# Kernel tuning notes

Hardware: AMD Instinct MI355X
Metric: run time of the kernel (lower is better)

## Reference

```python
import jax, jax.numpy as jnp
import numpy as np

B, S, H = 8, 1024, 768
NH, DH = 12, 64
F, E = 3072, 8
EPS = 1e-12

def layer_norm(x, g, b):
    mu = jnp.mean(x, axis=-1, keepdims=True)
    var = jnp.var(x, axis=-1, keepdims=True)
    return g * (x - mu) / jnp.sqrt(var + EPS) + b

def setup_inputs():
    key = jax.random.key(0)
    ks = jax.random.split(key, 20)
    std = 0.02
    d = {
        'hidden_states': jax.random.normal(ks[0], (B, S, H), jnp.float32),
        'Wq': jax.random.normal(ks[1], (H, H)) * std, 'bq': jnp.zeros((H,)),
        'Wk': jax.random.normal(ks[2], (H, H)) * std, 'bk': jnp.zeros((H,)),
        'Wv': jax.random.normal(ks[3], (H, H)) * std, 'bv': jnp.zeros((H,)),
        'Wao': jax.random.normal(ks[4], (H, H)) * std, 'bao': jnp.zeros((H,)),
        'ln1_g': jnp.ones((H,)), 'ln1_b': jnp.zeros((H,)),
        'Wr': jax.random.normal(ks[5], (H, E)) * std, 'br': jnp.zeros((E,)),
        'Wi': jax.random.normal(ks[6], (E, H, F)) * std, 'bi': jnp.zeros((E, F)),
        'Wo': jax.random.normal(ks[7], (F, H)) * std, 'bo': jnp.zeros((H,)),
        'ln2_g': jnp.ones((H,)), 'ln2_b': jnp.zeros((H,)),
    }
    return d

def reference(hidden_states, Wq, bq, Wk, bk, Wv, bv, Wao, bao, ln1_g, ln1_b,
              Wr, br, Wi, bi, Wo, bo, ln2_g, ln2_b):
    b, s, h = hidden_states.shape
    # --- self attention ---
    q = (hidden_states @ Wq + bq).reshape(b, s, NH, DH)
    k = (hidden_states @ Wk + bk).reshape(b, s, NH, DH)
    v = (hidden_states @ Wv + bv).reshape(b, s, NH, DH)
    scores = jnp.einsum('bqhd,bkhd->bhqk', q, k) / jnp.sqrt(jnp.float32(DH))
    probs = jax.nn.softmax(scores, axis=-1)
    ctx = jnp.einsum('bhqk,bkhd->bqhd', probs, v).reshape(b, s, h)
    attention_output = layer_norm(ctx @ Wao + bao + hidden_states, ln1_g, ln1_b)
    # --- router ---
    routing_scores = jax.nn.softmax(attention_output @ Wr + br, axis=-1)  # [b,s,E]
    routing_expert = jnp.argmax(routing_scores, axis=-1)  # [b,s]
    # --- expert FFN (dispatch/combine via per-expert masking) ---
    flat_x = attention_output.reshape(-1, h)          # [T,H]
    flat_e = routing_expert.reshape(-1)               # [T]
    flat_inter = jnp.zeros((b * s, F), flat_x.dtype)
    for e in range(E):
        mask = (flat_e == e)[:, None].astype(flat_x.dtype)
        y = jax.nn.gelu(flat_x @ Wi[e] + bi[e], approximate=False)
        flat_inter = flat_inter + mask * y
    inter = flat_inter.reshape(b, s, F)
    # --- output (dense + residual layernorm) ---
    layer_output = layer_norm(inter @ Wo + bo + attention_output, ln2_g, ln2_b)
    return layer_output, routing_scores
```

## Files before the change

### kernel.cpp

```cpp
#include <hip/hip_runtime.h>
#include <math.h>
#include <stdint.h>

#define TOKS 8192
#define HDIM 768
#define FDIM 3072
#define NEXP 8
#define NHEAD 12
#define SEQ 1024
#define BATCH 8
#define PERMSZ 9216

typedef __attribute__((ext_vector_type(8))) short s16x8;
typedef __attribute__((ext_vector_type(4))) short s16x4;
typedef __attribute__((ext_vector_type(4))) float f32x4;

__device__ __forceinline__ short f2bf(float f) {
  uint32_t u = __float_as_uint(f);
  uint32_t r = (u + 0x7fffu + ((u >> 16) & 1u)) >> 16;
  return (short)(r & 0xffffu);
}
__device__ __forceinline__ float bf2f(short h) {
  return __uint_as_float(((uint32_t)(uint16_t)h) << 16);
}
__device__ __forceinline__ void gload16(const void* g, void* l) {
  __builtin_amdgcn_global_load_lds(
      (const __attribute__((address_space(1))) uint32_t*)g,
      (__attribute__((address_space(3))) uint32_t*)l, 16, 0, 0);
}
__device__ __forceinline__ void pipe_wait_barrier() {
  asm volatile("s_waitcnt vmcnt(0)" ::: "memory");
  __builtin_amdgcn_s_barrier();
}

__global__ __launch_bounds__(256) void convert_split(
    const float* __restrict__ X, short* __restrict__ Xh, short* __restrict__ Xl, int n4)
{
  const int i = blockIdx.x * 256 + threadIdx.x;
  if (i >= n4) return;
  const float4 v = ((const float4*)X)[i];
  const float a[4] = {v.x, v.y, v.z, v.w};
  s16x4 h, l;
#pragma unroll
  for (int j = 0; j < 4; ++j) {
    h[j] = f2bf(a[j]);
    l[j] = f2bf(a[j] - bf2f(h[j]));
  }
  ((s16x4*)Xh)[i] = h;
  ((s16x4*)Xl)[i] = l;
}

__global__ __launch_bounds__(256) void transpose_split(
    const float* __restrict__ W, short* __restrict__ WTh, short* __restrict__ WTl,
    int K, int N)
{
  __shared__ float t[32][33];
  const int tid = threadIdx.x;
  const int tx = tid & 31, ty = tid >> 5;
  const int n0 = blockIdx.x * 32, k0 = blockIdx.y * 32;
#pragma unroll
  for (int r = 0; r < 4; ++r)
    t[ty + r * 8][tx] = W[(size_t)(k0 + ty + r * 8) * N + n0 + tx];
  __syncthreads();
#pragma unroll
  for (int r = 0; r < 4; ++r) {
    const float v = t[tx][ty + r * 8];
    const short h = f2bf(v);
    WTh[(size_t)(n0 + ty + r * 8) * K + k0 + tx] = h;
    WTl[(size_t)(n0 + ty + r * 8) * K + k0 + tx] = f2bf(v - bf2f(h));
  }
}

__global__ __launch_bounds__(256) void qkv_split_mfma(
    const short* __restrict__ Ah, const short* __restrict__ Al,
    const short* __restrict__ BhT, const short* __restrict__ BlT,
    const float* __restrict__ bias,
    short* __restrict__ QKh, short* __restrict__ QKl,
    short* __restrict__ VTh, short* __restrict__ VTl)
{
  const int K = 768;
  __shared__ __align__(16) short lAh[2][4096];
  __shared__ __align__(16) short lAl[2][4096];
  __shared__ __align__(16) short lBh[2][4096];
  __shared__ __align__(16) short lBl[2][4096];
  const int tid = threadIdx.x;
  const int w = tid >> 6, lane = tid & 63;
  const int wr = w >> 1, wc = w & 1;
  const int row0 = blockIdx.y * 128, col0 = blockIdx.x * 128;
  const int sr = lane & 15, kg = lane >> 4;
  const size_t a0 = (size_t)(row0 + 2 * w * 16 + sr) * K + kg * 8;
  const size_t a1 = a0 + (size_t)16 * K;
  const size_t b0 = (size_t)(col0 + 2 * w * 16 + sr) * K + kg * 8;
  const size_t b1 = b0 + (size_t)16 * K;
  const int d0 = (2 * w) * 512, d1 = (2 * w + 1) * 512;
#define STAGE_Q(bu, k0) do { \
    gload16(Ah + a0 + (k0), &lAh[bu][d0]); \
    gload16(Ah + a1 + (k0), &lAh[bu][d1]); \
    gload16(Al + a0 + (k0), &lAl[bu][d0]); \
    gload16(Al + a1 + (k0), &lAl[bu][d1]); \
    gload16(BhT + b0 + (k0), &lBh[bu][d0]); \
    gload16(BhT + b1 + (k0), &lBh[bu][d1]); \
    gload16(BlT + b0 + (k0), &lBl[bu][d0]); \
    gload16(BlT + b1 + (k0), &lBl[bu][d1]); \
  } while (0)
  f32x4 acc[4][4] = {};
  STAGE_Q(0, 0);
  pipe_wait_barrier();
  int cur = 0;
  for (int t = 0; t < 24; ++t) {
    if (t < 23) STAGE_Q(cur ^ 1, (t + 1) * 32);
    s16x8 ah[4], al[4], bh[4], bl[4];
#pragma unroll
    for (int i = 0; i < 4; ++i) {
      ah[i] = *(const s16x8*)&lAh[cur][(wr * 4 + i) * 512 + lane * 8];
      al[i] = *(const s16x8*)&lAl[cur][(wr * 4 + i) * 512 + lane * 8];
      bh[i] = *(const s16x8*)&lBh[cur][(wc * 4 + i) * 512 + lane * 8];
      bl[i] = *(const s16x8*)&lBl[cur][(wc * 4 + i) * 512 + lane * 8];
    }
#pragma unroll
    for (int mi = 0; mi < 4; ++mi)
#pragma unroll
      for (int ni = 0; ni < 4; ++ni) {
        acc[mi][ni] = __builtin_amdgcn_mfma_f32_16x16x32_bf16(ah[mi], bh[ni], acc[mi][ni], 0, 0, 0);
        acc[mi][ni] = __builtin_amdgcn_mfma_f32_16x16x32_bf16(ah[mi], bl[ni], acc[mi][ni], 0, 0, 0);
        acc[mi][ni] = __builtin_amdgcn_mfma_f32_16x16x32_bf16(al[mi], bh[ni], acc[mi][ni], 0, 0, 0);
      }
    pipe_wait_barrier();
    cur ^= 1;
  }
#undef STAGE_Q
  const int cl = lane & 15, rg = lane >> 4;
#pragma unroll
  for (int mi = 0; mi < 4; ++mi)
#pragma unroll
    for (int ni = 0; ni < 4; ++ni) {
      const int c = col0 + wc * 64 + ni * 16 + cl;
      const int rowb = row0 + wr * 64 + mi * 16 + rg * 4;
      s16x4 hv, lv;
#pragma unroll
      for (int r = 0; r < 4; ++r) {
        const float v = acc[mi][ni][r] + bias[c];
        const short hh = f2bf(v);
        hv[r] = hh;
        lv[r] = f2bf(v - bf2f(hh));
      }
      if (c < 1536) {
#pragma unroll
        for (int r = 0; r < 4; ++r) {
          QKh[(size_t)(rowb + r) * 1536 + c] = hv[r];
          QKl[(size_t)(rowb + r) * 1536 + c] = lv[r];
        }
      } else {
        const int dall = c - 1536;
        const size_t vi = (((size_t)((rowb >> 10) * NHEAD + (dall >> 6))) * 64 + (dall & 63)) * 1024
                          + (rowb & 1023);
        *(s16x4*)(VTh + vi) = hv;
        *(s16x4*)(VTl + vi) = lv;
      }
    }
}

__global__ __launch_bounds__(256) void gemm_splitk_staged(
    const short* __restrict__ Ah, const short* __restrict__ Al,
    const short* __restrict__ BhT, const short* __restrict__ BlT,
    const float* __restrict__ bias, float* __restrict__ C0, float* __restrict__ C1,
    int N, int K)
{
  __shared__ __align__(16) short lAh[2][4096];
  __shared__ __align__(16) short lAl[2][4096];
  __shared__ __align__(16) short lBh[2][4096];
  __shared__ __align__(16) short lBl[2][4096];
  const int tid = threadIdx.x;
  const int w = tid >> 6, lane = tid & 63;
  const int wr = w >> 1, wc = w & 1;
  const int row0 = blockIdx.y * 128, col0 = blockIdx.x * 128;
  const int z = blockIdx.z;
  const int Khalf = K >> 1, koff = z * Khalf;
  const int sr = lane & 15, kg = lane >> 4;
  const size_t a0 = (size_t)(row0 + 2 * w * 16 + sr) * K + koff + kg * 8;
  const size_t a1 = a0 + (size_t)16 * K;
  const size_t b0 = (size_t)(col0 + 2 * w * 16 + sr) * K + koff + kg * 8;
  const size_t b1 = b0 + (size_t)16 * K;
  const int d0 = (2 * w) * 512, d1 = (2 * w + 1) * 512;
#define STAGE_K4(bu, k0) do { \
    gload16(Ah + a0 + (k0), &lAh[bu][d0]); \
    gload16(Ah + a1 + (k0), &lAh[bu][d1]); \
    gload16(Al + a0 + (k0), &lAl[bu][d0]); \
    gload16(Al + a1 + (k0), &lAl[bu][d1]); \
    gload16(BhT + b0 + (k0), &lBh[bu][d0]); \
    gload16(BhT + b1 + (k0), &lBh[bu][d1]); \
    gload16(BlT + b0 + (k0), &lBl[bu][d0]); \
    gload16(BlT + b1 + (k0), &lBl[bu][d1]); \
  } while (0)
  f32x4 acc[4][4] = {};
  const int NT = Khalf >> 5;
  STAGE_K4(0, 0);
  pipe_wait_barrier();
  int cur = 0;
  for (int t = 0; t < NT; ++t) {
    if (t + 1 < NT) STAGE_K4(cur ^ 1, (t + 1) * 32);
    s16x8 ah[4], al[4], bh[4], bl[4];
#pragma unroll
    for (int i = 0; i < 4; ++i) {
      ah[i] = *(const s16x8*)&lAh[cur][(wr * 4 + i) * 512 + lane * 8];
      al[i] = *(const s16x8*)&lAl[cur][(wr * 4 + i) * 512 + lane * 8];
      bh[i] = *(const s16x8*)&lBh[cur][(wc * 4 + i) * 512 + lane * 8];
      bl[i] = *(const s16x8*)&lBl[cur][(wc * 4 + i) * 512 + lane * 8];
    }
#pragma unroll
    for (int mi = 0; mi < 4; ++mi)
#pragma unroll
      for (int ni = 0; ni < 4; ++ni) {
        acc[mi][ni] = __builtin_amdgcn_mfma_f32_16x16x32_bf16(ah[mi], bh[ni], acc[mi][ni], 0, 0, 0);
        acc[mi][ni] = __builtin_amdgcn_mfma_f32_16x16x32_bf16(ah[mi], bl[ni], acc[mi][ni], 0, 0, 0);
        acc[mi][ni] = __builtin_amdgcn_mfma_f32_16x16x32_bf16(al[mi], bh[ni], acc[mi][ni], 0, 0, 0);
      }
    pipe_wait_barrier();
    cur ^= 1;
  }
#undef STAGE_K4
  float* C = z ? C1 : C0;
  const int cl = lane & 15, rg = lane >> 4;
#pragma unroll
  for (int mi = 0; mi < 4; ++mi)
#pragma unroll
    for (int r = 0; r < 4; ++r) {
      const int row = row0 + wr * 64 + mi * 16 + rg * 4 + r;
#pragma unroll
      for (int ni = 0; ni < 4; ++ni) {
        const int c = col0 + wc * 64 + ni * 16 + cl;
        C[(size_t)row * N + c] = acc[mi][ni][r] + (z ? 0.f : bias[c]);
      }
    }
}

__global__ __launch_bounds__(256, 2) void attention_part(
    const short* __restrict__ QKh, const short* __restrict__ QKl,
    const short* __restrict__ VTh, const short* __restrict__ VTl,
    float* __restrict__ O0, float* __restrict__ O1,
    float2* __restrict__ ml0, float2* __restrict__ ml1)
{
  __shared__ __align__(16) short lPh[4][2560];
  __shared__ __align__(16) short lPl[4][2560];
  const int tid = threadIdx.x;
  const int w = tid >> 6, lane = tid & 63;
  const int b = blockIdx.z, h = blockIdx.y;
  const int z = blockIdx.x & 1;
  const int q0 = (blockIdx.x >> 1) * 128 + w * 32;
  const int kv0 = z * 512;
  const int sr = lane & 15, kg = lane >> 4;
  const int cl = sr, rg = kg;
  short* myPh = lPh[w];
  short* myPl = lPl[w];
  float* Op = z ? O1 : O0;
  float2* mlp = z ? ml1 : ml0;

  s16x8 qh[2][2], ql[2][2];
  {
    const size_t qbase = ((size_t)b * SEQ + q0 + sr) * 1536 + h * 64 + kg * 8;
#pragma unroll
    for (int mi = 0; mi < 2; ++mi)
#pragma unroll
      for (int ks = 0; ks < 2; ++ks) {
        const size_t o = qbase + (size_t)mi * (16 * 1536) + ks * 32;
        qh[mi][ks] = *(const s16x8*)(QKh + o);
        ql[mi][ks] = *(const s16x8*)(QKl + o);
      }
  }
  float m_run[2][4], l_run[2][4];
#pragma unroll
  for (int mi = 0; mi < 2; ++mi)
#pragma unroll
    for (int r = 0; r < 4; ++r) { m_run[mi][r] = -3.0e38f; l_run[mi][r] = 0.f; }
  f32x4 acc_o[2][4] = {};

  for (int kt = kv0; kt < kv0 + 512; kt += 64) {
    s16x8 kh[4][2], kl2[4][2];
    {
      const size_t kbase = ((size_t)b * SEQ + kt + sr) * 1536 + 768 + h * 64 + kg * 8;
#pragma unroll
      for (int ni = 0; ni < 4; ++ni)
#pragma unroll
        for (int ks = 0; ks < 2; ++ks) {
          const size_t o = kbase + (size_t)ni * (16 * 1536) + ks * 32;
          kh[ni][ks] = *(const s16x8*)(QKh + o);
          kl2[ni][ks] = *(const s16x8*)(QKl + o);
        }
    }
    f32x4 accs[2][4] = {};
#pragma unroll
    for (int ks = 0; ks < 2; ++ks)
#pragma unroll
      for (int ni = 0; ni < 4; ++ni)
#pragma unroll
        for (int mi = 0; mi < 2; ++mi) {
          accs[mi][ni] = __builtin_amdgcn_mfma_f32_16x16x32_bf16(qh[mi][ks], kh[ni][ks], accs[mi][ni], 0, 0, 0);
          accs[mi][ni] = __builtin_amdgcn_mfma_f32_16x16x32_bf16(qh[mi][ks], kl2[ni][ks], accs[mi][ni], 0, 0, 0);
          accs[mi][ni] = __builtin_amdgcn_mfma_f32_16x16x32_bf16(ql[mi][ks], kh[ni][ks], accs[mi][ni], 0, 0, 0);
        }
    s16x8 vh[4][2], vl2[4][2];
    {
      const size_t vbase = (((size_t)(b * NHEAD + h)) * 64 + sr) * 1024 + kt + kg * 8;
#pragma unroll
      for (int nd = 0; nd < 4; ++nd)
#pragma unroll
        for (int ks2 = 0; ks2 < 2; ++ks2) {
          const size_t o = vbase + (size_t)nd * (16 * 1024) + ks2 * 32;
          vh[nd][ks2] = *(const s16x8*)(VTh + o);
          vl2[nd][ks2] = *(const s16x8*)(VTl + o);
        }
    }
#pragma unroll
    for (int mi = 0; mi < 2; ++mi)
#pragma unroll
      for (int ni = 0; ni < 4; ++ni)
#pragma unroll
        for (int r = 0; r < 4; ++r)
          accs[mi][ni][r] *= 0.125f;
#pragma unroll
    for (int mi = 0; mi < 2; ++mi)
#pragma unroll
      for (int r = 0; r < 4; ++r) {
        float mx = fmaxf(fmaxf(accs[mi][0][r], accs[mi][1][r]),
                         fmaxf(accs[mi][2][r], accs[mi][3][r]));
        mx = fmaxf(mx, __shfl_xor(mx, 1));
        mx = fmaxf(mx, __shfl_xor(mx, 2));
        mx = fmaxf(mx, __shfl_xor(mx, 4));
        mx = fmaxf(mx, __shfl_xor(mx, 8));
        const float mn = fmaxf(m_run[mi][r], mx);
        const float c = __expf(m_run[mi][r] - mn);
        m_run[mi][r] = mn;
        l_run[mi][r] *= c;
#pragma unroll
        for (int nd = 0; nd < 4; ++nd) acc_o[mi][nd][r] *= c;
        float sum = 0.f;
#pragma unroll
        for (int ni = 0; ni < 4; ++ni) {
          const float p = __expf(accs[mi][ni][r] - mn);
          sum += p;
          const short hh = f2bf(p);
          const int idx = (mi * 2 + (ni >> 1)) * 640 + (rg * 4 + r) * 40 + (ni & 1) * 16 + cl;
          myPh[idx] = hh;
          myPl[idx] = f2bf(p - bf2f(hh));
        }
        sum += __shfl_xor(sum, 1);
        sum += __shfl_xor(sum, 2);
        sum += __shfl_xor(sum, 4);
        sum += __shfl_xor(sum, 8);
        l_run[mi][r] += sum;
      }
#pragma unroll
    for (int ks2 = 0; ks2 < 2; ++ks2) {
      s16x8 pf[2], pg[2];
#pragma unroll
      for (int mi = 0; mi < 2; ++mi) {
        const int ra = (mi * 2 + ks2) * 640 + sr * 40 + kg * 8;
        pf[mi] = *(const s16x8*)&myPh[ra];
        pg[mi] = *(const s16x8*)&myPl[ra];
      }
#pragma unroll
      for (int nd = 0; nd < 4; ++nd)
#pragma unroll
        for (int mi = 0; mi < 2; ++mi) {
          acc_o[mi][nd] = __builtin_amdgcn_mfma_f32_16x16x32_bf16(pf[mi], vh[nd][ks2], acc_o[mi][nd], 0, 0, 0);
          acc_o[mi][nd] = __builtin_amdgcn_mfma_f32_16x16x32_bf16(pf[mi], vl2[nd][ks2], acc_o[mi][nd], 0, 0, 0);
          acc_o[mi][nd] = __builtin_amdgcn_mfma_f32_16x16x32_bf16(pg[mi], vh[nd][ks2], acc_o[mi][nd], 0, 0, 0);
        }
    }
  }
#pragma unroll
  for (int mi = 0; mi < 2; ++mi)
#pragma unroll
    for (int nd = 0; nd < 4; ++nd)
#pragma unroll
      for (int r = 0; r < 4; ++r) {
        const int row = q0 + mi * 16 + rg * 4 + r;
        const int d = h * 64 + nd * 16 + cl;
        Op[((size_t)b * SEQ + row) * HDIM + d] = acc_o[mi][nd][r];
      }
  if (sr == 0) {
#pragma unroll
    for (int mi = 0; mi < 2; ++mi)
#pragma unroll
      for (int r = 0; r < 4; ++r) {
        const int row = q0 + mi * 16 + rg * 4 + r;
        mlp[(size_t)(b * NHEAD + h) * SEQ + row] = make_float2(m_run[mi][r], l_run[mi][r]);
      }
  }
}

__global__ __launch_bounds__(256) void combine_split(
    const float* __restrict__ O0, const float* __restrict__ O1,
    const float2* __restrict__ ml0, const float2* __restrict__ ml1,
    short* __restrict__ Ch, short* __restrict__ Cl)
{
  const int t = blockIdx.x;
  const int b = t >> 10, s = t & 1023;
  const int tid = threadIdx.x;
#pragma unroll
  for (int i = 0; i < 3; ++i) {
    const int idx = tid + i * 256;
    const int h = idx >> 6;
    const float2 a0 = ml0[(size_t)(b * NHEAD + h) * SEQ + s];
    const float2 a1 = ml1[(size_t)(b * NHEAD + h) * SEQ + s];
    const float mm = fmaxf(a0.x, a1.x);
    const float w0 = __expf(a0.x - mm), w1 = __expf(a1.x - mm);
    const float denom = a0.y * w0 + a1.y * w1;
    const size_t o = (size_t)t * HDIM + idx;
    const float v = (O0[o] * w0 + O1[o] * w1) / denom;
    const short hh = f2bf(v);
    Ch[o] = hh;
    Cl[o] = f2bf(v - bf2f(hh));
  }
}

__global__ __launch_bounds__(256) void convert_bf16(
    const float* __restrict__ X, short* __restrict__ Y, int n4)
{
  const int i = blockIdx.x * 256 + threadIdx.x;
  if (i >= n4) return;
  const float4 v = ((const float4*)X)[i];
  s16x4 s;
  s[0] = f2bf(v.x); s[1] = f2bf(v.y); s[2] = f2bf(v.z); s[3] = f2bf(v.w);
  ((s16x4*)Y)[i] = s;
}

__global__ __launch_bounds__(256) void transpose_to_bf16(
    const float* __restrict__ W, short* __restrict__ WT, int K, int N)
{
  const size_t off = (size_t)blockIdx.z * (size_t)K * N;
  const float* Wp = W + off;
  short* WTp = WT + off;
  __shared__ float t[32][33];
  const int tid = threadIdx.x;
  const int tx = tid & 31, ty = tid >> 5;
  const int n0 = blockIdx.x * 32, k0 = blockIdx.y * 32;
#pragma unroll
  for (int r = 0; r < 4; ++r)
    t[ty + r * 8][tx] = Wp[(size_t)(k0 + ty + r * 8) * N + n0 + tx];
  __syncthreads();
#pragma unroll
  for (int r = 0; r < 4; ++r)
    WTp[(size_t)(n0 + ty + r * 8) * K + k0 + tx] = f2bf(t[tx][ty + r * 8]);
}

__global__ __launch_bounds__(256) void expert_up_mfma(
    const short* __restrict__ Abf, const short* __restrict__ WiT,
    const float* __restrict__ bi, const int* __restrict__ perm,
    const int* __restrict__ offs, short* __restrict__ interb)
{
  const int row0 = blockIdx.x * 128;
  if (row0 >= offs[NEXP]) return;
  int e = 0;
  while (offs[e + 1] <= row0) ++e;
  __shared__ __align__(16) short lA[2][4096];
  __shared__ __align__(16) short lB[2][4096];
  __shared__ int toks[128];
  const int tid = threadIdx.x;
  const int w = tid >> 6, lane = tid & 63;
  const int wr = w >> 1, wc = w & 1;
  const int col0 = blockIdx.y * 128;
  if (tid < 128) toks[tid] = perm[row0 + tid];
  __syncthreads();
  const int sr = lane & 15, kg = lane >> 4;
  int t0 = toks[2 * w * 16 + sr];        if (t0 < 0) t0 = toks[0];
  int t1 = toks[(2 * w + 1) * 16 + sr];  if (t1 < 0) t1 = toks[0];
  const size_t a0 = (size_t)t0 * HDIM + kg * 8;
  const size_t a1 = (size_t)t1 * HDIM + kg * 8;
  const short* Bt = WiT + (size_t)e * FDIM * HDIM;
  const size_t b0 = (size_t)(col0 + 2 * w * 16 + sr) * HDIM + kg * 8;
  const size_t b1 = b0 + (size_t)16 * HDIM;
  const int d0 = (2 * w) * 512, d1 = (2 * w + 1) * 512;
#define STAGE_E(bu, k0) do { \
    gload16(Abf + a0 + (k0), &lA[bu][d0]); \
    gload16(Abf + a1 + (k0), &lA[bu][d1]); \
    gload16(Bt + b0 + (k0), &lB[bu][d0]); \
    gload16(Bt + b1 + (k0), &lB[bu][d1]); \
  } while (0)
  f32x4 acc[4][4] = {};
  STAGE_E(0, 0);
  pipe_wait_barrier();
  int cur = 0;
  for (int t = 0; t < 24; ++t) {
    if (t < 23) STAGE_E(cur ^ 1, (t + 1) * 32);
    s16x8 af[4], bg[4];
#pragma unroll
    for (int i = 0; i < 4; ++i) {
      af[i] = *(const s16x8*)&lA[cur][(wr * 4 + i) * 512 + lane * 8];
      bg[i] = *(const s16x8*)&lB[cur][(wc * 4 + i) * 512 + lane * 8];
    }
#pragma unroll
    for (int mi = 0; mi < 4; ++mi)
#pragma unroll
      for (int ni = 0; ni < 4; ++ni)
        acc[mi][ni] = __builtin_amdgcn_mfma_f32_16x16x32_bf16(af[mi], bg[ni], acc[mi][ni], 0, 0, 0);
    pipe_wait_barrier();
    cur ^= 1;
  }
#undef STAGE_E
  const int cl = lane & 15, rg = lane >> 4;
#pragma unroll
  for (int mi = 0; mi < 4; ++mi) {
#pragma unroll
    for (int r = 0; r < 4; ++r) {
      const int rl = wr * 64 + mi * 16 + rg * 4 + r;
      const int tok = toks[rl];
      if (tok < 0) continue;
#pragma unroll
      for (int ni = 0; ni < 4; ++ni) {
        const int c = col0 + wc * 64 + ni * 16 + cl;
        float v = acc[mi][ni][r] + bi[(size_t)e * FDIM + c];
        v = 0.5f * v * (1.0f + erff(v * 0.70710678118654752f));
        interb[(size_t)tok * FDIM + c] = f2bf(v);
      }
    }
  }
}

__global__ __launch_bounds__(256) void wo_mfma(
    const short* __restrict__ Ab, const short* __restrict__ BT,
    const float* __restrict__ bias, float* __restrict__ C0, float* __restrict__ C1)
{
  __shared__ __align__(16) short lA[2][4096];
  __shared__ __align__(16) short lB[2][4096];
  const int tid = threadIdx.x;
  const int w = tid >> 6, lane = tid & 63;
  const int wr = w >> 1, wc = w & 1;
  const int row0 = blockIdx.y * 128, col0 = blockIdx.x * 128;
  const int z = blockIdx.z;
  const int kbase = z * 1536;
  const int sr = lane & 15, kg = lane >> 4;
  const size_t a0 = (size_t)(row0 + 2 * w * 16 + sr) * FDIM + kbase + kg * 8;
  const size_t a1 = a0 + (size_t)16 * FDIM;
  const size_t b0 = (size_t)(col0 + 2 * w * 16 + sr) * FDIM + kbase + kg * 8;
  const size_t b1 = b0 + (size_t)16 * FDIM;
  const int d0 = (2 * w) * 512, d1 = (2 * w + 1) * 512;
#define STAGE_W(bu, k0) do { \
    gload16(Ab + a0 + (k0), &lA[bu][d0]); \
    gload16(Ab + a1 + (k0), &lA[bu][d1]); \
    gload16(BT + b0 + (k0), &lB[bu][d0]); \
    gload16(BT + b1 + (k0), &lB[bu][d1]); \
  } while (0)
  f32x4 acc[4][4] = {};
  STAGE_W(0, 0);
  pipe_wait_barrier();
  int cur = 0;
  for (int t = 0; t < 48; ++t) {
    if (t < 47) STAGE_W(cur ^ 1, (t + 1) * 32);
    s16x8 af[4], bg[4];
#pragma unroll
    for (int i = 0; i < 4; ++i) {
      af[i] = *(const s16x8*)&lA[cur][(wr * 4 + i) * 512 + lane * 8];
      bg[i] = *(const s16x8*)&lB[cur][(wc * 4 + i) * 512 + lane * 8];
    }
#pragma unroll
    for (int mi = 0; mi < 4; ++mi)
#pragma unroll
      for (int ni = 0; ni < 4; ++ni)
        acc[mi][ni] = __builtin_amdgcn_mfma_f32_16x16x32_bf16(af[mi], bg[ni], acc[mi][ni], 0, 0, 0);
    pipe_wait_barrier();
    cur ^= 1;
  }
#undef STAGE_W
  float* C = z ? C1 : C0;
  const int cl = lane & 15, rg = lane >> 4;
#pragma unroll
  for (int mi = 0; mi < 4; ++mi) {
#pragma unroll
    for (int r = 0; r < 4; ++r) {
      const int row = row0 + wr * 64 + mi * 16 + rg * 4 + r;
#pragma unroll
      for (int ni = 0; ni < 4; ++ni) {
        const int c = col0 + wc * 64 + ni * 16 + cl;
        C[(size_t)row * HDIM + c] = acc[mi][ni][r] + (z ? 0.f : bias[c]);
      }
    }
  }
}

__global__ __launch_bounds__(256) void add2_ln_kernel(
    const float* __restrict__ X1, const float* __restrict__ X2,
    const float* __restrict__ R, const float* __restrict__ g,
    const float* __restrict__ bb, float* __restrict__ out)
{
  const int t = blockIdx.x;
  const int tid = threadIdx.x;
  const float* x1 = X1 + (size_t)t * HDIM;
  const float* x2 = X2 + (size_t)t * HDIM;
  const float* r = R + (size_t)t * HDIM;
  float v[3];
  float sum = 0.f, ssq = 0.f;
#pragma unroll
  for (int i = 0; i < 3; ++i) {
    const float val = x1[tid + i * 256] + x2[tid + i * 256] + r[tid + i * 256];
    v[i] = val;
    sum += val;
    ssq += val * val;
  }
#pragma unroll
  for (int o = 32; o > 0; o >>= 1) {
    sum += __shfl_down(sum, o);
    ssq += __shfl_down(ssq, o);
  }
  __shared__ float red[10];
  const int wid = tid >> 6, lane = tid & 63;
  if (lane == 0) { red[wid] = sum; red[4 + wid] = ssq; }
  __syncthreads();
  if (tid == 0) {
    const float s = red[0] + red[1] + red[2] + red[3];
    const float q = red[4] + red[5] + red[6] + red[7];
    const float mean = s * (1.f / HDIM);
    const float var = q * (1.f / HDIM) - mean * mean;
    red[8] = mean;
    red[9] = rsqrtf(fmaxf(var, 0.f) + 1e-12f);
  }
  __syncthreads();
  const float mean = red[8], rstd = red[9];
#pragma unroll
  for (int i = 0; i < 3; ++i) {
    const int idx = tid + i * 256;
    out[(size_t)t * HDIM + idx] = g[idx] * (v[i] - mean) * rstd + bb[idx];
  }
}

__global__ __launch_bounds__(256) void router_kernel(
    const float* __restrict__ X, const float* __restrict__ Wr,
    const float* __restrict__ br, float* __restrict__ scores_out,
    int* __restrict__ expert, int* __restrict__ counts)
{
  const int wid = threadIdx.x >> 6, lane = threadIdx.x & 63;
  const int tok = blockIdx.x * 4 + wid;
  const float* x = X + (size_t)tok * HDIM;
  float acc[8] = {};
  for (int k0 = 0; k0 < HDIM; k0 += 64) {
    const float xv = x[k0 + lane];
    const float* wrow = Wr + (size_t)(k0 + lane) * NEXP;
    const float4 w0 = *reinterpret_cast<const float4*>(wrow);
    const float4 w1 = *reinterpret_cast<const float4*>(wrow + 4);
    acc[0] = fmaf(xv, w0.x, acc[0]);
    acc[1] = fmaf(xv, w0.y, acc[1]);
    acc[2] = fmaf(xv, w0.z, acc[2]);
    acc[3] = fmaf(xv, w0.w, acc[3]);
    acc[4] = fmaf(xv, w1.x, acc[4]);
    acc[5] = fmaf(xv, w1.y, acc[5]);
    acc[6] = fmaf(xv, w1.z, acc[6]);
    acc[7] = fmaf(xv, w1.w, acc[7]);
  }
#pragma unroll
  for (int e = 0; e < 8; ++e)
#pragma unroll
    for (int o = 32; o > 0; o >>= 1) acc[e] += __shfl_down(acc[e], o);
  if (lane == 0) {
    float mx = -3.0e38f;
#pragma unroll
    for (int e = 0; e < 8; ++e) { acc[e] += br[e]; mx = fmaxf(mx, acc[e]); }
    float sum = 0.f;
#pragma unroll
    for (int e = 0; e < 8; ++e) { acc[e] = expf(acc[e] - mx); sum += acc[e]; }
    const float inv = 1.f / sum;
    int best = 0;
    float bv = acc[0];
#pragma unroll
    for (int e = 0; e < 8; ++e) {
      const float p = acc[e] * inv;
      scores_out[(size_t)tok * NEXP + e] = p;
      if (acc[e] > bv) { bv = acc[e]; best = e; }
    }
    expert[tok] = best;
    atomicAdd(&counts[best], 1);
  }
}

__global__ void offsets_kernel(const int* __restrict__ counts, int* __restrict__ offs)
{
  if (threadIdx.x == 0 && blockIdx.x == 0) {
    int a = 0;
    for (int e = 0; e < NEXP; ++e) {
      offs[e] = a;
      a += ((counts[e] + 127) >> 7) << 7;
    }
    offs[NEXP] = a;
  }
}

__global__ __launch_bounds__(256) void scatter_kernel(
    const int* __restrict__ expert, const int* __restrict__ offs,
    int* __restrict__ cursor, int* __restrict__ perm)
{
  const int t = blockIdx.x * 256 + threadIdx.x;
  if (t >= TOKS) return;
  const int e = expert[t];
  const int pos = atomicAdd(&cursor[e], 1);
  perm[offs[e] + pos] = t;
}

extern "C" void kernel_launch(void* const* d_in, const int* in_sizes, int n_in,
                              void* d_out, int out_size, void* d_ws, size_t ws_size,
                              hipStream_t stream) {
  const float* hidden = (const float*)d_in[0];
  const float* Wq  = (const float*)d_in[1];
  const float* bq  = (const float*)d_in[2];
  const float* Wk  = (const float*)d_in[3];
  const float* bk  = (const float*)d_in[4];
  const float* Wv  = (const float*)d_in[5];
  const float* bv  = (const float*)d_in[6];
  const float* Wao = (const float*)d_in[7];
  const float* bao = (const float*)d_in[8];
  const float* ln1g = (const float*)d_in[9];
  const float* ln1b = (const float*)d_in[10];
  const float* Wr  = (const float*)d_in[11];
  const float* br  = (const float*)d_in[12];
  const float* Wi  = (const float*)d_in[13];
  const float* bi  = (const float*)d_in[14];
  const float* Wo  = (const float*)d_in[15];
  const float* bo  = (const float*)d_in[16];
  const float* ln2g = (const float*)d_in[17];
  const float* ln2b = (const float*)d_in[18];

  float* out = (float*)d_out;
  float* scores_out = out + (size_t)TOKS * HDIM;

  const size_t M1 = (size_t)TOKS * HDIM;
  const size_t HW = (size_t)HDIM * HDIM;
  float* ws = (float*)d_ws;
  short* QKhb = (short*)ws;
  short* QKlb = (short*)(ws + M1);
  short* VThb = (short*)(ws + 2 * M1);
  short* VTlb = VThb + (size_t)BATCH * NHEAD * 64 * 1024;
  float* O0b  = ws + 3 * M1;
  float* O1b  = ws + 4 * M1;
  float* bqkv = ws + 3 * M1;
  short* Hh = (short*)(ws + 4 * M1);
  short* Hl = Hh + M1;
  short* Ch = (short*)(ws + 2 * M1);
  short* Cl = Ch + M1;
  short* wt = (short*)(ws + 5 * M1);
  short* WqkvhT = wt;
  short* WqkvlT = wt + 3 * HW;
  short* WaohT  = wt + 6 * HW;
  short* WaolT  = wt + 7 * HW;
  float2* ml0 = (float2*)(ws + 5 * M1 + 4 * HW);
  float2* ml1 = ml0 + (size_t)BATCH * NHEAD * SEQ;
  float* aoproj0  = ws;
  float* aoproj1  = ws + 3 * M1;
  float* attn_out = ws + M1;
  float* tmp2a    = ws;
  float* tmp2b    = ws + 3 * M1;
  short* Abf    = (short*)(ws + 2 * M1);
  short* WiT    = Abf + M1;
  short* WoT    = WiT + (size_t)NEXP * FDIM * HDIM;
  short* interb = WoT + (size_t)HDIM * FDIM;
  int* ints   = (int*)(interb + (size_t)TOKS * FDIM);
  int* perm   = ints;
  int* expert = ints + PERMSZ;
  int* counts = expert + TOKS;
  int* offs   = counts + NEXP;
  int* cursor = offs + NEXP + 1;

  hipMemsetAsync(counts, 0, (NEXP + NEXP + 1 + NEXP) * sizeof(int), stream);
  hipMemsetAsync(perm, 0xFF, PERMSZ * sizeof(int), stream);
  hipMemcpyAsync(bqkv,        bq, HDIM * sizeof(float), hipMemcpyDeviceToDevice, stream);
  hipMemcpyAsync(bqkv + 768,  bk, HDIM * sizeof(float), hipMemcpyDeviceToDevice, stream);
  hipMemcpyAsync(bqkv + 1536, bv, HDIM * sizeof(float), hipMemcpyDeviceToDevice, stream);

  const dim3 blk(256);
  convert_split<<<dim3(TOKS * HDIM / 4 / 256), blk, 0, stream>>>(hidden, Hh, Hl, TOKS * HDIM / 4);
  transpose_split<<<dim3(24, 24), blk, 0, stream>>>(Wq,  WqkvhT,          WqkvlT,          HDIM, HDIM);
  transpose_split<<<dim3(24, 24), blk, 0, stream>>>(Wk,  WqkvhT + HW,     WqkvlT + HW,     HDIM, HDIM);
  transpose_split<<<dim3(24, 24), blk, 0, stream>>>(Wv,  WqkvhT + 2 * HW, WqkvlT + 2 * HW, HDIM, HDIM);
  transpose_split<<<dim3(24, 24), blk, 0, stream>>>(Wao, WaohT,           WaolT,           HDIM, HDIM);

  qkv_split_mfma<<<dim3(2304 / 128, TOKS / 128), blk, 0, stream>>>(
      Hh, Hl, WqkvhT, WqkvlT, bqkv, QKhb, QKlb, VThb, VTlb);

  attention_part<<<dim3((SEQ / 128) * 2, NHEAD, BATCH), blk, 0, stream>>>(
      QKhb, QKlb, VThb, VTlb, O0b, O1b, ml0, ml1);
  combine_split<<<dim3(TOKS), blk, 0, stream>>>(O0b, O1b, ml0, ml1, Ch, Cl);

  gemm_splitk_staged<<<dim3(HDIM / 128, TOKS / 128, 2), blk, 0, stream>>>(
      Ch, Cl, WaohT, WaolT, bao, aoproj0, aoproj1, HDIM, HDIM);
  add2_ln_kernel<<<dim3(TOKS), blk, 0, stream>>>(aoproj0, aoproj1, hidden, ln1g, ln1b, attn_out);

  router_kernel<<<dim3(TOKS / 4), blk, 0, stream>>>(attn_out, Wr, br, scores_out, expert, counts);
  offsets_kernel<<<dim3(1), dim3(64), 0, stream>>>(counts, offs);
  scatter_kernel<<<dim3(TOKS / 256), blk, 0, stream>>>(expert, offs, cursor, perm);

  transpose_to_bf16<<<dim3(FDIM / 32, HDIM / 32, NEXP), blk, 0, stream>>>(Wi, WiT, HDIM, FDIM);
  transpose_to_bf16<<<dim3(HDIM / 32, FDIM / 32, 1), blk, 0, stream>>>(Wo, WoT, FDIM, HDIM);
  convert_bf16<<<dim3(TOKS * HDIM / 4 / 256), blk, 0, stream>>>(attn_out, Abf, TOKS * HDIM / 4);

  expert_up_mfma<<<dim3(PERMSZ / 128, FDIM / 128), blk, 0, stream>>>(
      Abf, WiT, bi, perm, offs, interb);
  wo_mfma<<<dim3(HDIM / 128, TOKS / 128, 2), blk, 0, stream>>>(interb, WoT, bo, tmp2a, tmp2b);
  add2_ln_kernel<<<dim3(TOKS), blk, 0, stream>>>(tmp2a, tmp2b, attn_out, ln2g, ln2b, out);
}
```

Baseline: 907.8 us.

## Remap block indices for XCD-aware L2 locality and single-buffer A tiles in QKV GEMM

```diff
diff --git a/kernel.cpp b/kernel.cpp
--- a/kernel.cpp
+++ b/kernel.cpp
@@ -79,43 +79,53 @@
     short* __restrict__ VTh, short* __restrict__ VTl)
 {
   const int K = 768;
-  __shared__ __align__(16) short lAh[2][4096];
-  __shared__ __align__(16) short lAl[2][4096];
+  __shared__ __align__(16) short lAh[4096];
+  __shared__ __align__(16) short lAl[4096];
   __shared__ __align__(16) short lBh[2][4096];
   __shared__ __align__(16) short lBl[2][4096];
+  const int dsp = blockIdx.x + 18 * blockIdx.y;
+  const int orig = (dsp & 7) * 144 + (dsp >> 3);
+  const int bx = orig % 18, by = orig / 18;
   const int tid = threadIdx.x;
   const int w = tid >> 6, lane = tid & 63;
   const int wr = w >> 1, wc = w & 1;
-  const int row0 = blockIdx.y * 128, col0 = blockIdx.x * 128;
+  const int row0 = by * 128, col0 = bx * 128;
   const int sr = lane & 15, kg = lane >> 4;
   const size_t a0 = (size_t)(row0 + 2 * w * 16 + sr) * K + kg * 8;
   const size_t a1 = a0 + (size_t)16 * K;
   const size_t b0 = (size_t)(col0 + 2 * w * 16 + sr) * K + kg * 8;
   const size_t b1 = b0 + (size_t)16 * K;
   const int d0 = (2 * w) * 512, d1 = (2 * w + 1) * 512;
-#define STAGE_Q(bu, k0) do { \
-    gload16(Ah + a0 + (k0), &lAh[bu][d0]); \
-    gload16(Ah + a1 + (k0), &lAh[bu][d1]); \
-    gload16(Al + a0 + (k0), &lAl[bu][d0]); \
-    gload16(Al + a1 + (k0), &lAl[bu][d1]); \
+#define STAGE_QA(k0) do { \
+    gload16(Ah + a0 + (k0), &lAh[d0]); \
+    gload16(Ah + a1 + (k0), &lAh[d1]); \
+    gload16(Al + a0 + (k0), &lAl[d0]); \
+    gload16(Al + a1 + (k0), &lAl[d1]); \
+  } while (0)
+#define STAGE_QB(bu, k0) do { \
     gload16(BhT + b0 + (k0), &lBh[bu][d0]); \
     gload16(BhT + b1 + (k0), &lBh[bu][d1]); \
     gload16(BlT + b0 + (k0), &lBl[bu][d0]); \
     gload16(BlT + b1 + (k0), &lBl[bu][d1]); \
   } while (0)
   f32x4 acc[4][4] = {};
-  STAGE_Q(0, 0);
+  STAGE_QA(0);
+  STAGE_QB(0, 0);
   pipe_wait_barrier();
   int cur = 0;
   for (int t = 0; t < 24; ++t) {
-    if (t < 23) STAGE_Q(cur ^ 1, (t + 1) * 32);
     s16x8 ah[4], al[4], bh[4], bl[4];
 #pragma unroll
     for (int i = 0; i < 4; ++i) {
-      ah[i] = *(const s16x8*)&lAh[cur][(wr * 4 + i) * 512 + lane * 8];
-      al[i] = *(const s16x8*)&lAl[cur][(wr * 4 + i) * 512 + lane * 8];
+      ah[i] = *(const s16x8*)&lAh[(wr * 4 + i) * 512 + lane * 8];
+      al[i] = *(const s16x8*)&lAl[(wr * 4 + i) * 512 + lane * 8];
       bh[i] = *(const s16x8*)&lBh[cur][(wc * 4 + i) * 512 + lane * 8];
       bl[i] = *(const s16x8*)&lBl[cur][(wc * 4 + i) * 512 + lane * 8];
+    }
+    __syncthreads();
+    if (t < 23) {
+      STAGE_QA((t + 1) * 32);
+      STAGE_QB(cur ^ 1, (t + 1) * 32);
     }
 #pragma unroll
     for (int mi = 0; mi < 4; ++mi)
@@ -128,7 +138,8 @@
     pipe_wait_barrier();
     cur ^= 1;
   }
-#undef STAGE_Q
+#undef STAGE_QA
+#undef STAGE_QB
   const int cl = lane & 15, rg = lane >> 4;
 #pragma unroll
   for (int mi = 0; mi < 4; ++mi)
@@ -244,9 +255,12 @@
   __shared__ __align__(16) short lPl[4][2560];
   const int tid = threadIdx.x;
   const int w = tid >> 6, lane = tid & 63;
-  const int b = blockIdx.z, h = blockIdx.y;
-  const int z = blockIdx.x & 1;
-  const int q0 = (blockIdx.x >> 1) * 128 + w * 32;
+  const int dsp = blockIdx.x + 16 * (blockIdx.y + 12 * blockIdx.z);
+  const int orig = (dsp & 7) * 192 + (dsp >> 3);
+  const int wx = orig & 15;
+  const int b = orig / 192, h = (orig >> 4) % 12;
+  const int z = wx & 1;
+  const int q0 = (wx >> 1) * 128 + w * 32;
   const int kv0 = z * 512;
   const int sr = lane & 15, kg = lane >> 4;
   const int cl = sr, rg = kg;
```

New measurement: 861.9 us. -5.1%, faster.
